# Performance work log

Hardware: AMD Instinct MI355X
Metric: run time of the kernel (lower is better)

Reference implementation:

```python
import jax, jax.numpy as jnp
import numpy as np

N, NPG, BS = 32000, 1000, 32
E, H, L, R, K = 512000, 128, 3, 8, 64


def setup_inputs() -> dict:
    key = jax.random.key(0)
    ks = jax.random.split(key, 16)
    sc = 0.05
    x = jax.random.normal(ks[0], (N, H), jnp.float32)
    W_rel = jax.random.normal(ks[1], (L, R, H, H), jnp.float32) * sc
    W_self = jax.random.normal(ks[2], (L, H, H), jnp.float32) * sc
    rel_table = jax.random.normal(ks[3], (R, H), jnp.float32)
    Zn = jax.random.normal(ks[4], (K, H), jnp.float32) * sc
    proj_W = jax.random.normal(ks[5], (L * H, H), jnp.float32) * sc
    proj_b = jnp.zeros((H,), jnp.float32)
    fc_W = jax.random.normal(ks[6], (2 * L * H + 2 * H, 1), jnp.float32) * sc
    fc_b = jnp.zeros((1,), jnp.float32)
    rep_seq = jax.random.normal(ks[7], (BS, H), jnp.float32)
    src = jax.random.randint(ks[8], (E,), 0, N, jnp.int32)
    dst = jax.random.randint(ks[9], (E,), 0, N, jnp.int32)
    etype = jax.random.randint(ks[10], (E,), 0, R, jnp.int32)
    graph_id = (jnp.arange(N, dtype=jnp.int32) // NPG).astype(jnp.int32)
    head_ids = (jnp.arange(BS, dtype=jnp.int32) * NPG)           # node with id==1 per subgraph
    tail_ids = (jnp.arange(BS, dtype=jnp.int32) * NPG + 1)       # node with id==2 per subgraph
    rel_labels = jax.random.randint(ks[11], (BS,), 0, R, jnp.int32)
    return dict(x=x, W_rel=W_rel, W_self=W_self, rel_table=rel_table, Zn=Zn,
                proj_W=proj_W, proj_b=proj_b, fc_W=fc_W, fc_b=fc_b, rep_seq=rep_seq,
                src=src, dst=dst, etype=etype, graph_id=graph_id,
                head_ids=head_ids, tail_ids=tail_ids, rel_labels=rel_labels)


def reference(x, W_rel, W_self, rel_table, Zn, proj_W, proj_b, fc_W, fc_b, rep_seq,
              src, dst, etype, graph_id, head_ids, tail_ids, rel_labels):
    n, h_dim = x.shape
    bs = head_ids.shape[0]
    # RGCN message passing: aggregate src features per (dst, rel), then per-rel linear.
    seg = dst.astype(jnp.int32) * R + etype.astype(jnp.int32)  # [E]
    h = x
    reprs = []
    for l in range(L):
        agg = jax.ops.segment_sum(h[src], seg, num_segments=n * R)  # [N*R, H]
        agg = agg.reshape(n, R, h_dim)
        msg = jnp.einsum('nri,rio->no', agg, W_rel[l])
        h = jax.nn.relu(msg + h @ W_self[l])
        reprs.append(h)
    repr_ = jnp.stack(reprs, axis=1)  # [N, L, H]
    # mean_nodes pooling per subgraph
    counts = jax.ops.segment_sum(jnp.ones((n,), x.dtype), graph_id, num_segments=bs)
    g_mean = jax.ops.segment_sum(repr_, graph_id, num_segments=bs) / counts[:, None, None]
    g_out = jax.nn.leaky_relu(g_mean.reshape(bs, L * h_dim) @ proj_W + proj_b)  # [bs, H]
    # head/tail gathers
    head_flat = repr_[head_ids].reshape(bs, L * h_dim)
    tail_flat = repr_[tail_ids].reshape(bs, L * h_dim)
    rel_embs = rel_table[rel_labels]  # [bs, H]
    h_out = head_flat @ proj_W + proj_b
    t_out = tail_flat @ proj_W + proj_b
    # community view: cluster assignment (softmax) then summary (sigmoid)
    s1 = jax.nn.sigmoid(jax.nn.softmax(h_out @ Zn.T, axis=-1) @ Zn)
    s2 = jax.nn.sigmoid(jax.nn.softmax(t_out @ Zn.T, axis=-1) @ Zn)
    s = s1 * s2
    # view attention aggregation over [subgraph, sequence, community] views
    views = jnp.stack([g_out, rep_seq, s], axis=1)  # [bs, 3, H]
    att = jax.nn.softmax(jnp.sum(rel_embs[:, None, :] * views, axis=-1), axis=-1)  # [bs, 3]
    view_aggr = jnp.sum(att[:, :, None] * views, axis=1)  # [bs, H]
    # positive triplet scoring
    g_rep = jnp.concatenate([head_flat, tail_flat, rel_embs, view_aggr], axis=1)
    out_pos = g_rep @ fc_W + fc_b  # [bs, 1]
    return out_pos
```

## Files before the change

### kernel.cpp

```cpp
#include <hip/hip_runtime.h>

#define N_NODES 32000
#define NPG     1000
#define BSZ     32
#define NEDGE   512000
#define H       128
#define NL      3
#define NR      8
#define NW      1152

typedef __attribute__((ext_vector_type(8))) short short8;
typedef __attribute__((ext_vector_type(4))) float float4v;

__device__ __forceinline__ float bf2f(unsigned short u) {
  union { unsigned int i; float f; } v;
  v.i = ((unsigned int)u) << 16;
  return v.f;
}
__device__ __forceinline__ unsigned short f2bf(float f) {
  union { float f; unsigned int i; } v;
  v.f = f;
  unsigned int x = v.i;
  return (unsigned short)((x + 0x7FFFu + ((x >> 16) & 1u)) >> 16);
}

__global__ void k_count(const int* __restrict__ dst, int* __restrict__ cnt) {
  int e = blockIdx.x * blockDim.x + threadIdx.x;
  if (e < NEDGE) atomicAdd(&cnt[dst[e]], 1);
}

__global__ void k_scan(int* __restrict__ cursor, int* __restrict__ row_ptr) {
  __shared__ int ssum[256];
  __shared__ int soff[256];
  const int tid = threadIdx.x;
  const int CH = N_NODES / 256;
  const int base = tid * CH;
  int s = 0;
  for (int i = 0; i < CH; ++i) s += cursor[base + i];
  ssum[tid] = s;
  __syncthreads();
  if (tid == 0) {
    int r = 0;
    for (int i = 0; i < 256; ++i) { soff[i] = r; r += ssum[i]; }
    row_ptr[N_NODES] = r;
  }
  __syncthreads();
  int off = soff[tid];
  for (int i = 0; i < CH; ++i) {
    int c = cursor[base + i];
    row_ptr[base + i] = off;
    cursor[base + i] = off;
    off += c;
  }
}

__global__ void k_fill(const int* __restrict__ src, const int* __restrict__ dst,
                       const int* __restrict__ etype, int* __restrict__ cursor,
                       int* __restrict__ edge_off) {
  int e = blockIdx.x * blockDim.x + threadIdx.x;
  if (e < NEDGE) {
    int p = atomicAdd(&cursor[dst[e]], 1);
    edge_off[p] = src[e] * NW + etype[e] * H;
  }
}

__global__ void k_gcount(const int* __restrict__ graph_id, int* __restrict__ gcount) {
  __shared__ int hist[BSZ];
  const int t = threadIdx.x;
  if (t < BSZ) hist[t] = 0;
  __syncthreads();
  const int n = blockIdx.x * 256 + t;
  if (n < N_NODES) atomicAdd(&hist[graph_id[n]], 1);
  __syncthreads();
  if (t < BSZ) { int v = hist[t]; if (v) atomicAdd(&gcount[t], v); }
}

__global__ void k_cvtX(const float* __restrict__ x, unsigned short* __restrict__ hb) {
  const size_t i = ((size_t)blockIdx.x * blockDim.x + threadIdx.x) * 4;
  float4 v = *(const float4*)(x + i);
  ushort4 u = { f2bf(v.x), f2bf(v.y), f2bf(v.z), f2bf(v.w) };
  *(ushort4*)(hb + i) = u;
}

__global__ void k_cvtB(const float* __restrict__ W_rel, const float* __restrict__ W_self,
                       unsigned short* __restrict__ Bt) {
  const int t = blockIdx.x * blockDim.x + threadIdx.x;
  const int k = t & 127;
  const int n = (t >> 7) % NW;
  const int l = t / (NW * H);
  float v = (n < 1024) ? W_rel[(((size_t)l * NR + (n >> 7)) * H + k) * H + (n & 127)]
                       : W_self[((size_t)l * H + k) * H + (n - 1024)];
  Bt[(size_t)l * (NW * H) + (size_t)n * H + k] = f2bf(v);
}

__global__ __launch_bounds__(256) void k_gemm9(
    const unsigned short* __restrict__ Ah,
    const unsigned short* __restrict__ Bt,
    unsigned short* __restrict__ G)
{
  __shared__ unsigned short lds_a[128 * 136];
  __shared__ unsigned short lds_b[128 * 136];
  const int tid  = threadIdx.x;
  const int wave = tid >> 6, lane = tid & 63;
  const int l15 = lane & 15, quad = lane >> 4;
  const int m0 = blockIdx.x * 128;
  const int n0 = blockIdx.y * 128;
  const int mb = (wave & 1) * 64;
  const int nb = (wave >> 1) * 64;

  #pragma unroll
  for (int s = 0; s < 8; ++s) {
    int f  = s * 256 + tid;
    int m  = f >> 4;
    int ko = (f & 15) * 8;
    *(uint4*)(lds_a + m * 136 + ko) = *(const uint4*)(Ah + (size_t)(m0 + m) * H + ko);
    *(uint4*)(lds_b + m * 136 + ko) = *(const uint4*)(Bt + (size_t)(n0 + m) * H + ko);
  }
  __syncthreads();

  float4v acc[4][4];
  #pragma unroll
  for (int i = 0; i < 4; ++i)
    #pragma unroll
    for (int j = 0; j < 4; ++j) acc[i][j] = (float4v){0.f, 0.f, 0.f, 0.f};

  #pragma unroll
  for (int ks = 0; ks < 4; ++ks) {
    const int ko = ks * 32 + quad * 8;
    short8 afr[4], bfr[4];
    #pragma unroll
    for (int i = 0; i < 4; ++i)
      afr[i] = *(const short8*)(lds_a + (mb + i * 16 + l15) * 136 + ko);
    #pragma unroll
    for (int j = 0; j < 4; ++j)
      bfr[j] = *(const short8*)(lds_b + (nb + j * 16 + l15) * 136 + ko);
    #pragma unroll
    for (int i = 0; i < 4; ++i)
      #pragma unroll
      for (int j = 0; j < 4; ++j)
        acc[i][j] = __builtin_amdgcn_mfma_f32_16x16x32_bf16(afr[i], bfr[j], acc[i][j], 0, 0, 0);
  }

  __syncthreads();
  #pragma unroll
  for (int i = 0; i < 4; ++i)
    #pragma unroll
    for (int j = 0; j < 4; ++j)
      #pragma unroll
      for (int r = 0; r < 4; ++r)
        lds_a[(mb + i * 16 + quad * 4 + r) * 136 + nb + j * 16 + l15] = f2bf(acc[i][j][r]);
  __syncthreads();
  #pragma unroll
  for (int s = 0; s < 8; ++s) {
    int f  = s * 256 + tid;
    int m  = f >> 4;
    int ko = (f & 15) * 8;
    *(uint4*)(G + (size_t)(m0 + m) * NW + n0 + ko) = *(const uint4*)(lds_a + m * 136 + ko);
  }
}

__global__ __launch_bounds__(256) void k_gather(
    const unsigned short* __restrict__ G, const int* __restrict__ row_ptr,
    const int* __restrict__ edge_off, unsigned short* __restrict__ Hnext)
{
  const int node = blockIdx.x * 4 + (threadIdx.x >> 6);
  const int lane = threadIdx.x & 63;
  const int c0 = lane * 2;
  const int beg = row_ptr[node];
  const int end = row_ptr[node + 1];
  float sx, sy;
  {
    unsigned int u = *(const unsigned int*)(G + (size_t)node * NW + 1024 + c0);
    sx = bf2f((unsigned short)(u & 0xffff));
    sy = bf2f((unsigned short)(u >> 16));
  }
  int e = beg;
  for (; e + 8 <= end; e += 8) {
    int of[8]; unsigned int u[8];
    #pragma unroll
    for (int i = 0; i < 8; ++i) of[i] = edge_off[e + i];
    #pragma unroll
    for (int i = 0; i < 8; ++i)
      u[i] = *(const unsigned int*)(G + (size_t)of[i] + c0);
    #pragma unroll
    for (int i = 0; i < 8; ++i) {
      sx += bf2f((unsigned short)(u[i] & 0xffff));
      sy += bf2f((unsigned short)(u[i] >> 16));
    }
  }
  for (; e < end; ++e) {
    int of = edge_off[e];
    unsigned int u = *(const unsigned int*)(G + (size_t)of + c0);
    sx += bf2f((unsigned short)(u & 0xffff));
    sy += bf2f((unsigned short)(u >> 16));
  }
  sx = fmaxf(sx, 0.f);
  sy = fmaxf(sy, 0.f);
  *(unsigned int*)(Hnext + (size_t)node * H + c0) =
      (unsigned int)f2bf(sx) | ((unsigned int)f2bf(sy) << 16);
}

__global__ void k_gmean(const unsigned short* __restrict__ hb, float* __restrict__ gmean)
{
  const int g = blockIdx.x, l = blockIdx.y, c = blockIdx.z, t = threadIdx.x;
  const unsigned short* base =
      hb + ((size_t)(l + 1) * N_NODES + (size_t)g * NPG + (size_t)c * (NPG / 8)) * H + t * 2;
  float sx = 0.f, sy = 0.f;
  for (int i = 0; i < 125; ++i) {
    unsigned int u = *(const unsigned int*)(base + (size_t)i * H);
    sx += bf2f((unsigned short)(u & 0xffff));
    sy += bf2f((unsigned short)(u >> 16));
  }
  float* gp = gmean + (size_t)g * (NL * H) + l * H + t * 2;
  atomicAdd(gp, sx);
  atomicAdd(gp + 1, sy);
}

__global__ __launch_bounds__(128) void k_final(
    const unsigned short* __restrict__ hb, const float* __restrict__ gmean,
    const int* __restrict__ gcount,
    const float* __restrict__ rel_tb, const float* __restrict__ Zn,
    const float* __restrict__ projW, const float* __restrict__ projB,
    const float* __restrict__ fcW, const float* __restrict__ fcB,
    const float* __restrict__ repSeq,
    const int* __restrict__ head_ids, const int* __restrict__ tail_ids,
    const int* __restrict__ rel_lab, float* __restrict__ out)
{
  const int b = blockIdx.x;
  const int o = threadIdx.x;
  __shared__ float gm[384], hf[384], tf[384];
  __shared__ float go[128], ho[128], t_o[128], re[128], rs[128], sv[128];
  __shared__ float lg[128], pr[128], red[128], att[3];

  const int hid = head_ids[b], tlid = tail_ids[b], rl = rel_lab[b];
  const float cinv = 1.f / (float)gcount[b];
  #pragma unroll
  for (int l = 0; l < NL; ++l) {
    gm[l * H + o] = gmean[(size_t)b * (NL * H) + l * H + o] * cinv;
    hf[l * H + o] = bf2f(hb[((size_t)(l + 1) * N_NODES + hid) * H + o]);
    tf[l * H + o] = bf2f(hb[((size_t)(l + 1) * N_NODES + tlid) * H + o]);
  }
  re[o] = rel_tb[rl * H + o];
  rs[o] = repSeq[b * H + o];
  __syncthreads();

  float pb = projB[o];
  float sg = pb, sh = pb, st = pb;
  for (int i = 0; i < NL * H; ++i) {
    float wv = projW[i * H + o];
    sg = fmaf(gm[i], wv, sg);
    sh = fmaf(hf[i], wv, sh);
    st = fmaf(tf[i], wv, st);
  }
  go[o] = (sg > 0.f) ? sg : 0.01f * sg;
  ho[o] = sh;
  t_o[o] = st;
  __syncthreads();

  {
    const int k = o & 63;
    const float* v = (o < 64) ? ho : t_o;
    float s = 0.f;
    for (int i = 0; i < H; ++i) s = fmaf(v[i], Zn[k * H + i], s);
    lg[o] = s;
  }
  __syncthreads();
  if (o < 2) {
    float* l0 = &lg[o * 64];
    float* p0 = &pr[o * 64];
    float mx = l0[0];
    for (int k = 1; k < 64; ++k) mx = fmaxf(mx, l0[k]);
    float sum = 0.f;
    for (int k = 0; k < 64; ++k) { float e = __expf(l0[k] - mx); p0[k] = e; sum += e; }
    float inv = 1.f / sum;
    for (int k = 0; k < 64; ++k) p0[k] *= inv;
  }
  __syncthreads();
  {
    float s1 = 0.f, s2 = 0.f;
    for (int k = 0; k < 64; ++k) {
      float z = Zn[k * H + o];
      s1 = fmaf(pr[k], z, s1);
      s2 = fmaf(pr[64 + k], z, s2);
    }
    s1 = 1.f / (1.f + __expf(-s1));
    s2 = 1.f / (1.f + __expf(-s2));
    sv[o] = s1 * s2;
  }
  __syncthreads();
  if (o == 0) {
    float d0 = 0.f, d1 = 0.f, d2 = 0.f;
    for (int i = 0; i < H; ++i) { d0 += re[i] * go[i]; d1 += re[i] * rs[i]; d2 += re[i] * sv[i]; }
    float mx = fmaxf(d0, fmaxf(d1, d2));
    float e0 = __expf(d0 - mx), e1 = __expf(d1 - mx), e2 = __expf(d2 - mx);
    float inv = 1.f / (e0 + e1 + e2);
    att[0] = e0 * inv; att[1] = e1 * inv; att[2] = e2 * inv;
  }
  __syncthreads();
  float va = att[0] * go[o] + att[1] * rs[o] + att[2] * sv[o];

  float p = 0.f;
  p = fmaf(hf[o],       fcW[o],       p);
  p = fmaf(hf[128 + o], fcW[128 + o], p);
  p = fmaf(hf[256 + o], fcW[256 + o], p);
  p = fmaf(tf[o],       fcW[384 + o], p);
  p = fmaf(tf[128 + o], fcW[512 + o], p);
  p = fmaf(tf[256 + o], fcW[640 + o], p);
  p = fmaf(re[o],       fcW[768 + o], p);
  p = fmaf(va,          fcW[896 + o], p);
  red[o] = p;
  __syncthreads();
  if (o == 0) {
    float s = 0.f;
    for (int i = 0; i < 128; ++i) s += red[i];
    out[b] = s + fcB[0];
  }
}

extern "C" void kernel_launch(void* const* d_in, const int* in_sizes, int n_in,
                              void* d_out, int out_size, void* d_ws, size_t ws_size,
                              hipStream_t stream) {
  const float* x        = (const float*)d_in[0];
  const float* W_rel    = (const float*)d_in[1];
  const float* W_self   = (const float*)d_in[2];
  const float* rel_tb   = (const float*)d_in[3];
  const float* Zn       = (const float*)d_in[4];
  const float* proj_W   = (const float*)d_in[5];
  const float* proj_b   = (const float*)d_in[6];
  const float* fc_W     = (const float*)d_in[7];
  const float* fc_b     = (const float*)d_in[8];
  const float* rep_seq  = (const float*)d_in[9];
  const int* src      = (const int*)d_in[10];
  const int* dst      = (const int*)d_in[11];
  const int* etype    = (const int*)d_in[12];
  const int* graph_id = (const int*)d_in[13];
  const int* head_ids = (const int*)d_in[14];
  const int* tail_ids = (const int*)d_in[15];
  const int* rel_lab  = (const int*)d_in[16];
  float* out = (float*)d_out;

  char* w = (char*)d_ws;
  unsigned short* G  = (unsigned short*)w; w += (size_t)N_NODES * NW * 2;
  unsigned short* hb = (unsigned short*)w; w += (size_t)(NL + 1) * N_NODES * H * 2;
  unsigned short* Bt = (unsigned short*)w; w += (size_t)NL * NW * H * 2;
  int* row_ptr  = (int*)w;  w += (size_t)32004 * 4;
  int* edge_off = (int*)w;  w += (size_t)NEDGE * 4;
  char* z = w;
  int* cursor  = (int*)w;   w += (size_t)N_NODES * 4;
  int* gcount  = (int*)w;   w += (size_t)32 * 4;
  float* gmean = (float*)w; w += (size_t)BSZ * NL * H * 4;
  size_t zbytes = (size_t)(w - z);

  hipMemsetAsync(z, 0, zbytes, stream);
  k_count <<<NEDGE / 256, 256, 0, stream>>>(dst, cursor);
  k_scan  <<<1, 256, 0, stream>>>(cursor, row_ptr);
  k_fill  <<<NEDGE / 256, 256, 0, stream>>>(src, dst, etype, cursor, edge_off);
  k_gcount<<<(N_NODES + 255) / 256, 256, 0, stream>>>(graph_id, gcount);
  k_cvtX  <<<(N_NODES * H) / (256 * 4), 256, 0, stream>>>(x, hb);
  k_cvtB  <<<(NL * NW * H) / 256, 256, 0, stream>>>(W_rel, W_self, Bt);

  for (int l = 0; l < NL; ++l) {
    const unsigned short* hp = hb + (size_t)l * N_NODES * H;
    unsigned short* hn = hb + (size_t)(l + 1) * N_NODES * H;
    k_gemm9 <<<dim3(N_NODES / 128, 9), 256, 0, stream>>>(hp, Bt + (size_t)l * NW * H, G);
    k_gather<<<N_NODES / 4, 256, 0, stream>>>(G, row_ptr, edge_off, hn);
  }
  k_gmean<<<dim3(BSZ, NL, 8), 64, 0, stream>>>(hb, gmean);
  k_final<<<BSZ, H, 0, stream>>>(hb, gmean, gcount, rel_tb, Zn, proj_W, proj_b, fc_W, fc_b,
                                 rep_seq, head_ids, tail_ids, rel_lab, out);
  (void)in_sizes; (void)n_in; (void)out_size; (void)ws_size;
}
```

Before: 384.9 us.

## Fuse prep kernels, parallelize CSR scan, fold graph mean into gather

Merges the bf16 conversion of x and the weights, the in-degree count and the graph-size histogram into one multi-role prep kernel. The single-block serial prefix scan is replaced by a three-kernel parallel scan over a padded bin array. The separate graph-mean reduction kernel is removed: each gather thread instead atomically adds its post-ReLU values into the per-graph accumulator. That last change trades a small kernel for heavily contended float atomics, since about 1000 nodes hit the same addresses per graph. It also makes the sums' accumulation order nondeterministic.

```diff
diff --git a/kernel.cpp b/kernel.cpp
--- a/kernel.cpp
+++ b/kernel.cpp
@@ -8,6 +8,7 @@
 #define NL      3
 #define NR      8
 #define NW      1152
+#define NBIN    32768
 
 typedef __attribute__((ext_vector_type(8))) short short8;
 typedef __attribute__((ext_vector_type(4))) float float4v;
@@ -24,34 +25,90 @@
   return (unsigned short)((x + 0x7FFFu + ((x >> 16) & 1u)) >> 16);
 }
 
-__global__ void k_count(const int* __restrict__ dst, int* __restrict__ cnt) {
-  int e = blockIdx.x * blockDim.x + threadIdx.x;
-  if (e < NEDGE) atomicAdd(&cnt[dst[e]], 1);
-}
-
-__global__ void k_scan(int* __restrict__ cursor, int* __restrict__ row_ptr) {
-  __shared__ int ssum[256];
-  __shared__ int soff[256];
-  const int tid = threadIdx.x;
-  const int CH = N_NODES / 256;
-  const int base = tid * CH;
-  int s = 0;
-  for (int i = 0; i < CH; ++i) s += cursor[base + i];
-  ssum[tid] = s;
-  __syncthreads();
-  if (tid == 0) {
+__global__ __launch_bounds__(256) void k_prep(
+    const float* __restrict__ x, const float* __restrict__ W_rel,
+    const float* __restrict__ W_self, const int* __restrict__ dst,
+    const int* __restrict__ graph_id,
+    unsigned short* __restrict__ hb, unsigned short* __restrict__ Bt,
+    int* __restrict__ cnt, int* __restrict__ gcount)
+{
+  const int b = blockIdx.x, t = threadIdx.x;
+  if (b < 4000) {
+    const size_t i = ((size_t)b * 256 + t) * 4;
+    float4 v = *(const float4*)(x + i);
+    ushort4 u = { f2bf(v.x), f2bf(v.y), f2bf(v.z), f2bf(v.w) };
+    *(ushort4*)(hb + i) = u;
+  } else if (b < 5728) {
+    const int g = (b - 4000) * 256 + t;
+    const int k = g & 127;
+    const int n = (g >> 7) % NW;
+    const int l = g / (NW * H);
+    float v = (n < 1024) ? W_rel[(((size_t)l * NR + (n >> 7)) * H + k) * H + (n & 127)]
+                         : W_self[((size_t)l * H + k) * H + (n - 1024)];
+    Bt[(size_t)l * (NW * H) + (size_t)n * H + k] = f2bf(v);
+  } else if (b < 7728) {
+    const int e = (b - 5728) * 256 + t;
+    atomicAdd(&cnt[dst[e]], 1);
+  } else {
+    __shared__ int hist[BSZ];
+    if (t < BSZ) hist[t] = 0;
+    __syncthreads();
+    const int n = (b - 7728) * 256 + t;
+    if (n < N_NODES) atomicAdd(&hist[graph_id[n]], 1);
+    __syncthreads();
+    if (t < BSZ) { int v = hist[t]; if (v) atomicAdd(&gcount[t], v); }
+  }
+}
+
+__global__ __launch_bounds__(256) void k_scanA(const int* __restrict__ cnt,
+                                               int* __restrict__ bsum) {
+  __shared__ int red[256];
+  const int t = threadIdx.x;
+  int4 v = *(const int4*)(cnt + blockIdx.x * 1024 + t * 4);
+  red[t] = v.x + v.y + v.z + v.w;
+  __syncthreads();
+  for (int off = 128; off > 0; off >>= 1) {
+    if (t < off) red[t] += red[t + off];
+    __syncthreads();
+  }
+  if (t == 0) bsum[blockIdx.x] = red[0];
+}
+
+__global__ __launch_bounds__(64) void k_scanB(const int* __restrict__ bsum,
+                                              int* __restrict__ boff) {
+  const int t = threadIdx.x;
+  __shared__ int v[64];
+  v[t] = (t < 32) ? bsum[t] : 0;
+  __syncthreads();
+  if (t == 0) {
     int r = 0;
-    for (int i = 0; i < 256; ++i) { soff[i] = r; r += ssum[i]; }
-    row_ptr[N_NODES] = r;
-  }
-  __syncthreads();
-  int off = soff[tid];
-  for (int i = 0; i < CH; ++i) {
-    int c = cursor[base + i];
-    row_ptr[base + i] = off;
-    cursor[base + i] = off;
-    off += c;
-  }
+    for (int i = 0; i < 32; ++i) { int c = v[i]; v[i] = r; r += c; }
+  }
+  __syncthreads();
+  if (t < 32) boff[t] = v[t];
+}
+
+__global__ __launch_bounds__(256) void k_scanC(const int* __restrict__ cnt,
+                                               const int* __restrict__ boff,
+                                               int* __restrict__ row_ptr,
+                                               int* __restrict__ cursor) {
+  __shared__ int ts[256];
+  const int t = threadIdx.x;
+  const int base = blockIdx.x * 1024 + t * 4;
+  int4 v = *(const int4*)(cnt + base);
+  const int s = v.x + v.y + v.z + v.w;
+  ts[t] = s;
+  __syncthreads();
+  for (int off = 1; off < 256; off <<= 1) {
+    int val = (t >= off) ? ts[t - off] : 0;
+    __syncthreads();
+    ts[t] += val;
+    __syncthreads();
+  }
+  int ex = ts[t] - s + boff[blockIdx.x];
+  int4 w = { ex, ex + v.x, ex + v.x + v.y, ex + v.x + v.y + v.z };
+  *(int4*)(row_ptr + base) = w;
+  *(int4*)(cursor + base) = w;
 }
 
 __global__ void k_fill(const int* __restrict__ src, const int* __restrict__ dst,
@@ -62,35 +119,6 @@
     int p = atomicAdd(&cursor[dst[e]], 1);
     edge_off[p] = src[e] * NW + etype[e] * H;
   }
-}
-
-__global__ void k_gcount(const int* __restrict__ graph_id, int* __restrict__ gcount) {
-  __shared__ int hist[BSZ];
-  const int t = threadIdx.x;
-  if (t < BSZ) hist[t] = 0;
-  __syncthreads();
-  const int n = blockIdx.x * 256 + t;
-  if (n < N_NODES) atomicAdd(&hist[graph_id[n]], 1);
-  __syncthreads();
-  if (t < BSZ) { int v = hist[t]; if (v) atomicAdd(&gcount[t], v); }
-}
-
-__global__ void k_cvtX(const float* __restrict__ x, unsigned short* __restrict__ hb) {
-  const size_t i = ((size_t)blockIdx.x * blockDim.x + threadIdx.x) * 4;
-  float4 v = *(const float4*)(x + i);
-  ushort4 u = { f2bf(v.x), f2bf(v.y), f2bf(v.z), f2bf(v.w) };
-  *(ushort4*)(hb + i) = u;
-}
-
-__global__ void k_cvtB(const float* __restrict__ W_rel, const float* __restrict__ W_self,
-                       unsigned short* __restrict__ Bt) {
-  const int t = blockIdx.x * blockDim.x + threadIdx.x;
-  const int k = t & 127;
-  const int n = (t >> 7) % NW;
-  const int l = t / (NW * H);
-  float v = (n < 1024) ? W_rel[(((size_t)l * NR + (n >> 7)) * H + k) * H + (n & 127)]
-                       : W_self[((size_t)l * H + k) * H + (n - 1024)];
-  Bt[(size_t)l * (NW * H) + (size_t)n * H + k] = f2bf(v);
 }
 
 __global__ __launch_bounds__(256) void k_gemm9(
@@ -161,7 +189,8 @@
 
 __global__ __launch_bounds__(256) void k_gather(
     const unsigned short* __restrict__ G, const int* __restrict__ row_ptr,
-    const int* __restrict__ edge_off, unsigned short* __restrict__ Hnext)
+    const int* __restrict__ edge_off, const int* __restrict__ graph_id,
+    unsigned short* __restrict__ Hnext, float* __restrict__ gmean, int l)
 {
   const int node = blockIdx.x * 4 + (threadIdx.x >> 6);
   const int lane = threadIdx.x & 63;
@@ -196,24 +225,11 @@
   }
   sx = fmaxf(sx, 0.f);
   sy = fmaxf(sy, 0.f);
+  float* gp = gmean + (size_t)graph_id[node] * (NL * H) + l * H + c0;
+  atomicAdd(gp, sx);
+  atomicAdd(gp + 1, sy);
   *(unsigned int*)(Hnext + (size_t)node * H + c0) =
       (unsigned int)f2bf(sx) | ((unsigned int)f2bf(sy) << 16);
-}
-
-__global__ void k_gmean(const unsigned short* __restrict__ hb, float* __restrict__ gmean)
-{
-  const int g = blockIdx.x, l = blockIdx.y, c = blockIdx.z, t = threadIdx.x;
-  const unsigned short* base =
-      hb + ((size_t)(l + 1) * N_NODES + (size_t)g * NPG + (size_t)c * (NPG / 8)) * H + t * 2;
-  float sx = 0.f, sy = 0.f;
-  for (int i = 0; i < 125; ++i) {
-    unsigned int u = *(const unsigned int*)(base + (size_t)i * H);
-    sx += bf2f((unsigned short)(u & 0xffff));
-    sy += bf2f((unsigned short)(u >> 16));
-  }
-  float* gp = gmean + (size_t)g * (NL * H) + l * H + t * 2;
-  atomicAdd(gp, sx);
-  atomicAdd(gp + 1, sy);
 }
 
 __global__ __launch_bounds__(128) void k_final(
@@ -343,29 +359,29 @@
   unsigned short* G  = (unsigned short*)w; w += (size_t)N_NODES * NW * 2;
   unsigned short* hb = (unsigned short*)w; w += (size_t)(NL + 1) * N_NODES * H * 2;
   unsigned short* Bt = (unsigned short*)w; w += (size_t)NL * NW * H * 2;
-  int* row_ptr  = (int*)w;  w += (size_t)32004 * 4;
+  int* row_ptr  = (int*)w;  w += (size_t)NBIN * 4;
   int* edge_off = (int*)w;  w += (size_t)NEDGE * 4;
+  int* bsum     = (int*)w;  w += (size_t)64 * 4;
+  int* boff     = (int*)w;  w += (size_t)64 * 4;
   char* z = w;
-  int* cursor  = (int*)w;   w += (size_t)N_NODES * 4;
+  int* cursor  = (int*)w;   w += (size_t)NBIN * 4;
   int* gcount  = (int*)w;   w += (size_t)32 * 4;
   float* gmean = (float*)w; w += (size_t)BSZ * NL * H * 4;
   size_t zbytes = (size_t)(w - z);
 
   hipMemsetAsync(z, 0, zbytes, stream);
-  k_count <<<NEDGE / 256, 256, 0, stream>>>(dst, cursor);
-  k_scan  <<<1, 256, 0, stream>>>(cursor, row_ptr);
-  k_fill  <<<NEDGE / 256, 256, 0, stream>>>(src, dst, etype, cursor, edge_off);
-  k_gcount<<<(N_NODES + 255) / 256, 256, 0, stream>>>(graph_id, gcount);
-  k_cvtX  <<<(N_NODES * H) / (256 * 4), 256, 0, stream>>>(x, hb);
-  k_cvtB  <<<(NL * NW * H) / 256, 256, 0, stream>>>(W_rel, W_self, Bt);
+  k_prep <<<7853, 256, 0, stream>>>(x, W_rel, W_self, dst, graph_id, hb, Bt, cursor, gcount);
+  k_scanA<<<NBIN / 1024, 256, 0, stream>>>(cursor, bsum);
+  k_scanB<<<1, 64, 0, stream>>>(bsum, boff);
+  k_scanC<<<NBIN / 1024, 256, 0, stream>>>(cursor, boff, row_ptr, cursor);
+  k_fill <<<NEDGE / 256, 256, 0, stream>>>(src, dst, etype, cursor, edge_off);
 
   for (int l = 0; l < NL; ++l) {
     const unsigned short* hp = hb + (size_t)l * N_NODES * H;
     unsigned short* hn = hb + (size_t)(l + 1) * N_NODES * H;
     k_gemm9 <<<dim3(N_NODES / 128, 9), 256, 0, stream>>>(hp, Bt + (size_t)l * NW * H, G);
-    k_gather<<<N_NODES / 4, 256, 0, stream>>>(G, row_ptr, edge_off, hn);
-  }
-  k_gmean<<<dim3(BSZ, NL, 8), 64, 0, stream>>>(hb, gmean);
+    k_gather<<<N_NODES / 4, 256, 0, stream>>>(G, row_ptr, edge_off, graph_id, hn, gmean, l);
+  }
   k_final<<<BSZ, H, 0, stream>>>(hb, gmean, gcount, rel_tb, Zn, proj_W, proj_b, fc_W, fc_b,
                                  rep_seq, head_ids, tail_ids, rel_lab, out);
   (void)in_sizes; (void)n_in; (void)out_size; (void)ws_size;
```

Measured after the change: 675.9 us. 1.76x slower.
